# Kernel tuning notes

Hardware: AMD Instinct MI355X
Metric: run time of the kernel (lower is better)

The kernel has to match this reference:

```python
import jax, jax.numpy as jnp
import numpy as np

H = 50   # hidden_dim (hardcoded in module)
D = 16   # input_dim
B = 4096
T = 512

def _uniform(key, shape, k):
    return jax.random.uniform(key, shape, jnp.float32, -k, k)

def setup_inputs() -> dict:
    key = jax.random.key(0)
    ks = jax.random.split(key, 12)
    k = 1.0 / np.sqrt(H)  # PyTorch LSTM/Linear init bound
    return {
        "x": jax.random.normal(ks[0], (B, T, D), jnp.float32),
        "W_ih0": _uniform(ks[1], (4 * H, D), k),
        "W_hh0": _uniform(ks[2], (4 * H, H), k),
        "b_ih0": _uniform(ks[3], (4 * H,), k),
        "b_hh0": _uniform(ks[4], (4 * H,), k),
        "W_ih1": _uniform(ks[5], (4 * H, H), k),
        "W_hh1": _uniform(ks[6], (4 * H, H), k),
        "b_ih1": _uniform(ks[7], (4 * H,), k),
        "b_hh1": _uniform(ks[8], (4 * H,), k),
        "W_fc": _uniform(ks[9], (1, H), k),
        "b_fc": _uniform(ks[10], (1,), k),
    }

def _lstm_layer(x_tbd, W_ih, W_hh, b):
    # x_tbd: [T, B, Din]; returns (ys [T,B,H], h_final [B,H])
    Bsz = x_tbd.shape[1]
    # precompute input projections for all timesteps: [T, B, 4H]
    xproj = jnp.einsum('tbd,gd->tbg', x_tbd, W_ih) + b

    def step(carry, xp):
        h, c = carry
        gates = xp + h @ W_hh.T  # [B, 4H]
        i, f, g, o = jnp.split(gates, 4, axis=-1)  # torch gate order i,f,g,o
        i = jax.nn.sigmoid(i)
        f = jax.nn.sigmoid(f)
        g = jnp.tanh(g)
        o = jax.nn.sigmoid(o)
        c = f * c + i * g
        h = o * jnp.tanh(c)
        return (h, c), h

    init = (jnp.zeros((Bsz, H), x_tbd.dtype), jnp.zeros((Bsz, H), x_tbd.dtype))
    (h_fin, _), ys = jax.lax.scan(step, init, xproj)
    return ys, h_fin

def reference(x, W_ih0, W_hh0, b_ih0, b_hh0, W_ih1, W_hh1, b_ih1, b_hh1, W_fc, b_fc):
    x_tbd = jnp.transpose(x, (1, 0, 2))  # [T, B, D]
    ys0, _ = _lstm_layer(x_tbd, W_ih0, W_hh0, b_ih0 + b_hh0)
    _, h_n = _lstm_layer(ys0, W_ih1, W_hh1, b_ih1 + b_hh1)
    return h_n @ W_fc.T + b_fc  # [B, 1]
```

## Files before the change

kernel.cpp:

```cpp
#include <hip/hip_runtime.h>


#define TSTEPS 512
#define DIN 16
#define HID 50
#define BPB 16

typedef _Float16 half8 __attribute__((ext_vector_type(8)));
typedef __fp16 fp16x2 __attribute__((ext_vector_type(2)));
typedef float f32x4 __attribute__((ext_vector_type(4)));
typedef float f32x2 __attribute__((ext_vector_type(2)));

#define MF(A, B, C) __builtin_amdgcn_mfma_f32_16x16x32_f16((A), (B), (C), 0, 0, 0)

#define HBUF 2304
#define H0_O 0
#define H1_O 4608
#define SH_BYTES 9216

#define BAR() asm volatile("s_waitcnt lgkmcnt(0)\ns_barrier" ::: "memory")

#define NL2E  (-1.4426950408889634f)
#define P2L2E (2.8853900817779268f)

__device__ __forceinline__ unsigned pack2h(float a, float b) {
  union { fp16x2 h; unsigned u; } pk;
  pk.h = __builtin_amdgcn_cvt_pkrtz(a, b);
  return pk.u;
}

__device__ __forceinline__ f32x2 cell2p(const f32x4 gA, const f32x4 gB, f32x2& C) {
  f32x2 gi = {gA[0], gB[0]}, gf = {gA[1], gB[1]};
  f32x2 gg = {gA[2], gB[2]}, go = {gA[3], gB[3]};
  f32x2 ei, ef, eg, eo;
  ei[0] = __builtin_amdgcn_exp2f(gi[0]); ei[1] = __builtin_amdgcn_exp2f(gi[1]);
  ef[0] = __builtin_amdgcn_exp2f(gf[0]); ef[1] = __builtin_amdgcn_exp2f(gf[1]);
  eg[0] = __builtin_amdgcn_exp2f(gg[0]); eg[1] = __builtin_amdgcn_exp2f(gg[1]);
  eo[0] = __builtin_amdgcn_exp2f(go[0]); eo[1] = __builtin_amdgcn_exp2f(go[1]);
  const f32x2 one = {1.f, 1.f};
  const f32x2 c2 = {P2L2E, P2L2E};
  f32x2 a = one + ei, f = one + ef, b = one + eg;
  f32x2 ab = a * b;
  f32x2 f2 = ef * c2 + c2;
  f32x2 t = (eg - one) * f2 + C * ab;
  f32x2 p = f * ab;
  f32x2 rp;
  rp[0] = __builtin_amdgcn_rcpf(p[0]);
  rp[1] = __builtin_amdgcn_rcpf(p[1]);
  C = t * rp;
  f32x2 ec;
  ec[0] = __builtin_amdgcn_exp2f(fminf(C[0], 30.f));
  ec[1] = __builtin_amdgcn_exp2f(fminf(C[1], 30.f));
  f32x2 q = (one + eo) * (one + ec);
  float r2 = __builtin_amdgcn_rcpf(q[0] * q[1]);
  f32x2 h;
  h[0] = (ec[0] - 1.f) * (r2 * q[1]);
  h[1] = (ec[1] - 1.f) * (r2 * q[0]);
  return h;
}

__device__ __forceinline__ half8 load_wfrag(const float* __restrict__ W, int kld,
                                            bool permk, int kreal, int gt, int kt,
                                            int lane, float scale) {
  const int gp = 16 * gt + (lane & 15);
  const int u = gp >> 2, j = gp & 3;
  const int kb = kt * 32 + (lane >> 4) * 8;
  half8 f;
#pragma unroll
  for (int i = 0; i < 8; ++i) {
    const int p = kb + i;
    const int kk = permk ? ((p & ~7) + (((p & 1) << 2) | ((p >> 1) & 3))) : p;
    float v = (u < HID && kk < kreal) ? W[(j * HID + u) * kld + kk] : 0.f;
    f[i] = (_Float16)(v * scale);
  }
  return f;
}

#define LOADX(R0, R1, TT)                                                      \
  do {                                                                         \
    int tl_ = (TT);                                                            \
    if (tl_ > TSTEPS - 1) tl_ = TSTEPS - 1;                                    \
    const float* p_ = xcol + (size_t)tl_ * DIN;                                \
    (R0) = *(const float4*)p_;                                                 \
    (R1) = *(const float4*)(p_ + 4);                                           \
  } while (0)

#define BXB(BX, R0, R1)                                                        \
  do {                                                                         \
    union { half8 h8; fp16x2 p2[4]; } u_;                                      \
    u_.p2[0] = __builtin_amdgcn_cvt_pkrtz((R0).x, (R0).y);                     \
    u_.p2[1] = __builtin_amdgcn_cvt_pkrtz((R0).z, (R0).w);                     \
    u_.p2[2] = __builtin_amdgcn_cvt_pkrtz((R1).x, (R1).y);                     \
    u_.p2[3] = __builtin_amdgcn_cvt_pkrtz((R1).z, (R1).w);                     \
    (BX) = u_.h8;                                                              \
  } while (0)

extern "C" __global__ void __launch_bounds__(512, 2)
lstm2_v11(const float* __restrict__ x,
          const float* __restrict__ Wih0, const float* __restrict__ Whh0,
          const float* __restrict__ bih0, const float* __restrict__ bhh0,
          const float* __restrict__ Wih1, const float* __restrict__ Whh1,
          const float* __restrict__ bih1, const float* __restrict__ bhh1,
          const float* __restrict__ Wfc, const float* __restrict__ bfc,
          float* __restrict__ out) {
  __shared__ __align__(16) char sh[SH_BYTES];
  const int tid = threadIdx.x;
  const int lane = tid & 63;
  const int wv = tid >> 6;
  const int bcol = lane & 15;
  const int kg = lane >> 4;
  const int bbase = blockIdx.x * BPB;

  const int nt = (wv < 5) ? 2 : 1;
  const int gt0 = (wv < 5) ? 2 * wv : (10 + (wv - 5));

  const float* xcol = x + ((size_t)(bbase + bcol)) * TSTEPS * DIN + (kg & 1) * 8;

  for (int i = tid; i < SH_BYTES / 4; i += 512) ((int*)sh)[i] = 0;

  const float wsc = ((lane & 3) == 2) ? P2L2E : NL2E;
  half8 w0x[2], w0h[2][2], w1i[2][2], w1h[2][2];
  f32x4 bias0v[2] = {{0,0,0,0},{0,0,0,0}}, bias1v[2] = {{0,0,0,0},{0,0,0,0}};
#pragma unroll
  for (int gi = 0; gi < 2; ++gi) {
    if (gi < nt) {
      const int gt = gt0 + gi;
      w0x[gi] = load_wfrag(Wih0, DIN, false, DIN, gt, 0, lane, wsc);
#pragma unroll
      for (int kt = 0; kt < 2; ++kt) {
        w0h[gi][kt] = load_wfrag(Whh0, HID, true, HID, gt, kt, lane, wsc);
        w1i[gi][kt] = load_wfrag(Wih1, HID, true, HID, gt, kt, lane, wsc);
        w1h[gi][kt] = load_wfrag(Whh1, HID, true, HID, gt, kt, lane, wsc);
      }
      const int u = 4 * gt + kg;
      if (u < HID) {
#pragma unroll
        for (int j = 0; j < 4; ++j) {
          const float bs = (j == 2) ? P2L2E : NL2E;
          bias0v[gi][j] = bs * (bih0[j * HID + u] + bhh0[j * HID + u]);
          bias1v[gi][j] = bs * (bih1[j * HID + u] + bhh1[j * HID + u]);
        }
      }
    }
  }

  f32x2 C0 = {0.f, 0.f}, C1 = {0.f, 0.f};
  const int hoff = bcol * 144 + kg * 16;
  const int wo = (nt == 2) ? (bcol * 144 + (gt0 >> 1) * 16 + kg * 4)
                           : (bcol * 144 + (8 * (gt0 >> 1) + 2 * kg + (gt0 & 1)) * 2);

  BAR();

  float4 a0, a1, b0, b1;
  LOADX(a0, a1, 0);
  half8 bx0;
  BXB(bx0, a0, a1);
  LOADX(a0, a1, 1);
  LOADX(b0, b1, 2);
  {
    f32x4 r0 = MF(w0x[0], bx0, bias0v[0]);
    if (nt == 2) {
      f32x4 r1 = MF(w0x[1], bx0, bias0v[1]);
      f32x2 H = cell2p(r0, r1, C0);
      *(unsigned*)(sh + H0_O + wo) = pack2h(H[0], H[1]);
    } else {
      f32x2 Cp = {0.f, 0.f};
      f32x2 H = cell2p(r0, r0, Cp);
      *(_Float16*)(sh + H0_O + wo) = (_Float16)H[0];
      C0[0] = 0.f;
      C0[1] = Cp[0];
    }
  }
  BAR();

#define STEP2(P, BX)                                                           \
  do {                                                                         \
    half8 bh0[2], bh1[2];                                                      \
    _Pragma("unroll") for (int kt = 0; kt < 2; ++kt) {                         \
      bh0[kt] = *(const half8*)(sh + H0_O + (P)*HBUF + hoff + kt * 64);        \
      bh1[kt] = *(const half8*)(sh + H1_O + (P)*HBUF + hoff + kt * 64);        \
    }                                                                          \
    const f32x4 z = {0.f, 0.f, 0.f, 0.f};                                      \
    f32x4 tq0a = MF(w1i[0][0], bh0[0], bias1v[0]);                             \
    tq0a = MF(w1h[0][0], bh1[0], tq0a);                                        \
    f32x4 tq0b = MF(w1i[0][1], bh0[1], z);                                     \
    tq0b = MF(w1h[0][1], bh1[1], tq0b);                                        \
    f32x4 qv0 = tq0a + tq0b;                                                   \
    f32x4 tq1a = MF(w1i[1][0], bh0[0], bias1v[1]);                             \
    tq1a = MF(w1h[1][0], bh1[0], tq1a);                                        \
    f32x4 tq1b = MF(w1i[1][1], bh0[1], z);                                     \
    tq1b = MF(w1h[1][1], bh1[1], tq1b);                                        \
    f32x4 qv1 = tq1a + tq1b;                                                   \
    f32x4 tr0a = MF(w0x[0], (BX), bias0v[0]);                                  \
    tr0a = MF(w0h[0][0], bh0[0], tr0a);                                        \
    f32x4 tr0b = MF(w0h[0][1], bh0[1], z);                                     \
    f32x4 rv0 = tr0a + tr0b;                                                   \
    f32x4 tr1a = MF(w0x[1], (BX), bias0v[1]);                                  \
    tr1a = MF(w0h[1][0], bh0[0], tr1a);                                        \
    f32x4 tr1b = MF(w0h[1][1], bh0[1], z);                                     \
    f32x4 rv1 = tr1a + tr1b;                                                   \
    f32x2 H1 = cell2p(qv0, qv1, C1);                                           \
    *(unsigned*)(sh + H1_O + ((P) ^ 1) * HBUF + wo) = pack2h(H1[0], H1[1]);    \
    f32x2 H0 = cell2p(rv0, rv1, C0);                                           \
    *(unsigned*)(sh + H0_O + ((P) ^ 1) * HBUF + wo) = pack2h(H0[0], H0[1]);    \
  } while (0)

#define STEP1(P, BX)                                                           \
  do {                                                                         \
    half8 bh0[2], bh1[2];                                                      \
    _Pragma("unroll") for (int kt = 0; kt < 2; ++kt) {                         \
      bh0[kt] = *(const half8*)(sh + H0_O + (P)*HBUF + hoff + kt * 64);        \
      bh1[kt] = *(const half8*)(sh + H1_O + (P)*HBUF + hoff + kt * 64);        \
    }                                                                          \
    const f32x4 z = {0.f, 0.f, 0.f, 0.f};                                      \
    f32x4 tqa = MF(w1i[0][0], bh0[0], bias1v[0]);                              \
    tqa = MF(w1h[0][0], bh1[0], tqa);                                          \
    f32x4 tqb = MF(w1i[0][1], bh0[1], z);                                      \
    tqb = MF(w1h[0][1], bh1[1], tqb);                                          \
    f32x4 qv = tqa + tqb;                                                      \
    f32x4 tra = MF(w0x[0], (BX), bias0v[0]);                                   \
    tra = MF(w0h[0][0], bh0[0], tra);                                          \
    f32x4 trb = MF(w0h[0][1], bh0[1], z);                                      \
    f32x4 rv = tra + trb;                                                      \
    f32x2 H = cell2p(qv, rv, C0);                                              \
    *(_Float16*)(sh + H1_O + ((P) ^ 1) * HBUF + wo) = (_Float16)H[0];          \
    *(_Float16*)(sh + H0_O + ((P) ^ 1) * HBUF + wo) = (_Float16)H[1];          \
  } while (0)

  for (int s = 0; s < TSTEPS; s += 2) {
    {
      half8 bxA;
      BXB(bxA, a0, a1);
      LOADX(a0, a1, s + 3);
      if (nt == 2) { STEP2(0, bxA); } else { STEP1(0, bxA); }
    }
    BAR();
    {
      half8 bxB;
      BXB(bxB, b0, b1);
      LOADX(b0, b1, s + 4);
      if (nt == 2) { STEP2(1, bxB); } else { STEP1(1, bxB); }
    }
    BAR();
  }

  if (tid < BPB) {
    float acc = bfc[0];
#pragma unroll 10
    for (int u = 0; u < HID; ++u) {
      const int pp = (u & ~7) + 2 * (u & 3) + ((u >> 2) & 1);
      float h = (float)(*(const _Float16*)(sh + H1_O + tid * 144 + pp * 2));
      acc = fmaf(Wfc[u], h, acc);
    }
    out[bbase + tid] = acc;
  }
}

extern "C" void kernel_launch(void* const* d_in, const int* in_sizes, int n_in,
                              void* d_out, int out_size, void* d_ws, size_t ws_size,
                              hipStream_t stream) {
  (void)in_sizes; (void)n_in; (void)d_ws; (void)ws_size; (void)out_size;
  lstm2_v11<<<dim3(4096 / BPB), dim3(512), 0, stream>>>(
      (const float*)d_in[0], (const float*)d_in[1], (const float*)d_in[2],
      (const float*)d_in[3], (const float*)d_in[4], (const float*)d_in[5],
      (const float*)d_in[6], (const float*)d_in[7], (const float*)d_in[8],
      (const float*)d_in[9], (const float*)d_in[10], (float*)d_out);
}
```

Measured before the change: 370.3 us.

## Shrink LSTM block to four waves, each handling three or four gate tiles

Cuts the block from 8 waves to 4. Each wave now owns 3 or 4 gate tiles (wave 0 owns tiles 0-3), so the 13 tiles are covered with fewer waves and the per-step barrier is cheaper. The MFMA accumulation chains are merged into single serial chains instead of split partial sums. In exchange, each wave carries more weight registers and does a longer serial MFMA chain per step, and launch bounds move to 256 threads with 1 block minimum.

```diff
diff --git a/kernel.cpp b/kernel.cpp
--- a/kernel.cpp
+++ b/kernel.cpp
@@ -95,8 +95,8 @@
     (BX) = u_.h8;                                                              \
   } while (0)
 
-extern "C" __global__ void __launch_bounds__(512, 2)
-lstm2_v11(const float* __restrict__ x,
+extern "C" __global__ void __launch_bounds__(256, 1)
+lstm2_v13(const float* __restrict__ x,
           const float* __restrict__ Wih0, const float* __restrict__ Whh0,
           const float* __restrict__ bih0, const float* __restrict__ bhh0,
           const float* __restrict__ Wih1, const float* __restrict__ Whh1,
@@ -111,43 +111,52 @@
   const int kg = lane >> 4;
   const int bbase = blockIdx.x * BPB;
 
-  const int nt = (wv < 5) ? 2 : 1;
-  const int gt0 = (wv < 5) ? 2 * wv : (10 + (wv - 5));
+  const int gA = (wv == 0) ? 0 : (wv == 1) ? 4 : (wv == 2) ? 8 : 10;
+  const int gS = (wv == 1) ? 6 : (wv == 2) ? 7 : 12;
 
   const float* xcol = x + ((size_t)(bbase + bcol)) * TSTEPS * DIN + (kg & 1) * 8;
 
-  for (int i = tid; i < SH_BYTES / 4; i += 512) ((int*)sh)[i] = 0;
+  for (int i = tid; i < SH_BYTES / 4; i += 256) ((int*)sh)[i] = 0;
 
   const float wsc = ((lane & 3) == 2) ? P2L2E : NL2E;
-  half8 w0x[2], w0h[2][2], w1i[2][2], w1h[2][2];
-  f32x4 bias0v[2] = {{0,0,0,0},{0,0,0,0}}, bias1v[2] = {{0,0,0,0},{0,0,0,0}};
-#pragma unroll
-  for (int gi = 0; gi < 2; ++gi) {
-    if (gi < nt) {
-      const int gt = gt0 + gi;
-      w0x[gi] = load_wfrag(Wih0, DIN, false, DIN, gt, 0, lane, wsc);
-#pragma unroll
-      for (int kt = 0; kt < 2; ++kt) {
-        w0h[gi][kt] = load_wfrag(Whh0, HID, true, HID, gt, kt, lane, wsc);
-        w1i[gi][kt] = load_wfrag(Wih1, HID, true, HID, gt, kt, lane, wsc);
-        w1h[gi][kt] = load_wfrag(Whh1, HID, true, HID, gt, kt, lane, wsc);
-      }
-      const int u = 4 * gt + kg;
-      if (u < HID) {
-#pragma unroll
-        for (int j = 0; j < 4; ++j) {
-          const float bs = (j == 2) ? P2L2E : NL2E;
-          bias0v[gi][j] = bs * (bih0[j * HID + u] + bhh0[j * HID + u]);
-          bias1v[gi][j] = bs * (bih1[j * HID + u] + bhh1[j * HID + u]);
+  half8 w0x[4], w0h[4][2], w1i[4][2], w1h[4][2];
+  f32x4 bias0v[4] = {{0,0,0,0},{0,0,0,0},{0,0,0,0},{0,0,0,0}};
+  f32x4 bias1v[4] = {{0,0,0,0},{0,0,0,0},{0,0,0,0},{0,0,0,0}};
+  {
+    int gts[4];
+    gts[0] = gA; gts[1] = gA + 1;
+    gts[2] = (wv == 0) ? 2 : gS;
+    gts[3] = 3;
+    const int nslot = (wv == 0) ? 4 : 3;
+#pragma unroll
+    for (int si = 0; si < 4; ++si) {
+      if (si < nslot) {
+        const int gt = gts[si];
+        w0x[si] = load_wfrag(Wih0, DIN, false, DIN, gt, 0, lane, wsc);
+#pragma unroll
+        for (int kt = 0; kt < 2; ++kt) {
+          w0h[si][kt] = load_wfrag(Whh0, HID, true, HID, gt, kt, lane, wsc);
+          w1i[si][kt] = load_wfrag(Wih1, HID, true, HID, gt, kt, lane, wsc);
+          w1h[si][kt] = load_wfrag(Whh1, HID, true, HID, gt, kt, lane, wsc);
+        }
+        const int u = 4 * gt + kg;
+        if (u < HID) {
+#pragma unroll
+          for (int j = 0; j < 4; ++j) {
+            const float bs = (j == 2) ? P2L2E : NL2E;
+            bias0v[si][j] = bs * (bih0[j * HID + u] + bhh0[j * HID + u]);
+            bias1v[si][j] = bs * (bih1[j * HID + u] + bhh1[j * HID + u]);
+          }
         }
       }
     }
   }
 
-  f32x2 C0 = {0.f, 0.f}, C1 = {0.f, 0.f};
+  f32x2 C0a = {0.f, 0.f}, C1a = {0.f, 0.f}, C0b = {0.f, 0.f}, C1b = {0.f, 0.f};
   const int hoff = bcol * 144 + kg * 16;
-  const int wo = (nt == 2) ? (bcol * 144 + (gt0 >> 1) * 16 + kg * 4)
-                           : (bcol * 144 + (8 * (gt0 >> 1) + 2 * kg + (gt0 & 1)) * 2);
+  const int wo_p1 = bcol * 144 + (gA >> 1) * 16 + kg * 4;
+  const int wo_p2 = bcol * 144 + 16 + kg * 4;
+  const int wo_s  = bcol * 144 + (8 * (gS >> 1) + 2 * kg + (gS & 1)) * 2;
 
   BAR();
 
@@ -159,72 +168,70 @@
   LOADX(b0, b1, 2);
   {
     f32x4 r0 = MF(w0x[0], bx0, bias0v[0]);
-    if (nt == 2) {
-      f32x4 r1 = MF(w0x[1], bx0, bias0v[1]);
-      f32x2 H = cell2p(r0, r1, C0);
-      *(unsigned*)(sh + H0_O + wo) = pack2h(H[0], H[1]);
+    f32x4 r1 = MF(w0x[1], bx0, bias0v[1]);
+    f32x2 H = cell2p(r0, r1, C0a);
+    *(unsigned*)(sh + H0_O + wo_p1) = pack2h(H[0], H[1]);
+    if (wv == 0) {
+      f32x4 r2 = MF(w0x[2], bx0, bias0v[2]);
+      f32x4 r3 = MF(w0x[3], bx0, bias0v[3]);
+      f32x2 H2 = cell2p(r2, r3, C0b);
+      *(unsigned*)(sh + H0_O + wo_p2) = pack2h(H2[0], H2[1]);
     } else {
-      f32x2 Cp = {0.f, 0.f};
-      f32x2 H = cell2p(r0, r0, Cp);
-      *(_Float16*)(sh + H0_O + wo) = (_Float16)H[0];
-      C0[0] = 0.f;
-      C0[1] = Cp[0];
+      f32x4 rs = MF(w0x[2], bx0, bias0v[2]);
+      f32x2 Ct = {0.f, 0.f};
+      f32x2 Hs = cell2p(rs, rs, Ct);
+      *(_Float16*)(sh + H0_O + wo_s) = (_Float16)Hs[0];
+      C0b[0] = 0.f;
+      C0b[1] = Ct[0];
     }
   }
   BAR();
 
-#define STEP2(P, BX)                                                           \
+#define QCHAIN(QV, SI)                                                         \
+  f32x4 QV = MF(w1i[SI][0], bh0[0], bias1v[SI]);                               \
+  QV = MF(w1h[SI][0], bh1[0], QV);                                             \
+  QV = MF(w1i[SI][1], bh0[1], QV);                                             \
+  QV = MF(w1h[SI][1], bh1[1], QV)
+#define RCHAIN(RV, SI, BX)                                                     \
+  f32x4 RV = MF(w0x[SI], (BX), bias0v[SI]);                                    \
+  RV = MF(w0h[SI][0], bh0[0], RV);                                             \
+  RV = MF(w0h[SI][1], bh0[1], RV)
+
+#define STEP(P, BX)                                                            \
   do {                                                                         \
     half8 bh0[2], bh1[2];                                                      \
     _Pragma("unroll") for (int kt = 0; kt < 2; ++kt) {                         \
       bh0[kt] = *(const half8*)(sh + H0_O + (P)*HBUF + hoff + kt * 64);        \
       bh1[kt] = *(const half8*)(sh + H1_O + (P)*HBUF + hoff + kt * 64);        \
     }                                                                          \
-    const f32x4 z = {0.f, 0.f, 0.f, 0.f};                                      \
-    f32x4 tq0a = MF(w1i[0][0], bh0[0], bias1v[0]);                             \
-    tq0a = MF(w1h[0][0], bh1[0], tq0a);                                        \
-    f32x4 tq0b = MF(w1i[0][1], bh0[1], z);                                     \
-    tq0b = MF(w1h[0][1], bh1[1], tq0b);                                        \
-    f32x4 qv0 = tq0a + tq0b;                                                   \
-    f32x4 tq1a = MF(w1i[1][0], bh0[0], bias1v[1]);                             \
-    tq1a = MF(w1h[1][0], bh1[0], tq1a);                                        \
-    f32x4 tq1b = MF(w1i[1][1], bh0[1], z);                                     \
-    tq1b = MF(w1h[1][1], bh1[1], tq1b);                                        \
-    f32x4 qv1 = tq1a + tq1b;                                                   \
-    f32x4 tr0a = MF(w0x[0], (BX), bias0v[0]);                                  \
-    tr0a = MF(w0h[0][0], bh0[0], tr0a);                                        \
-    f32x4 tr0b = MF(w0h[0][1], bh0[1], z);                                     \
-    f32x4 rv0 = tr0a + tr0b;                                                   \
-    f32x4 tr1a = MF(w0x[1], (BX), bias0v[1]);                                  \
-    tr1a = MF(w0h[1][0], bh0[0], tr1a);                                        \
-    f32x4 tr1b = MF(w0h[1][1], bh0[1], z);                                     \
-    f32x4 rv1 = tr1a + tr1b;                                                   \
-    f32x2 H1 = cell2p(qv0, qv1, C1);                                           \
-    *(unsigned*)(sh + H1_O + ((P) ^ 1) * HBUF + wo) = pack2h(H1[0], H1[1]);    \
-    f32x2 H0 = cell2p(rv0, rv1, C0);                                           \
-    *(unsigned*)(sh + H0_O + ((P) ^ 1) * HBUF + wo) = pack2h(H0[0], H0[1]);    \
-  } while (0)
-
-#define STEP1(P, BX)                                                           \
-  do {                                                                         \
-    half8 bh0[2], bh1[2];                                                      \
-    _Pragma("unroll") for (int kt = 0; kt < 2; ++kt) {                         \
-      bh0[kt] = *(const half8*)(sh + H0_O + (P)*HBUF + hoff + kt * 64);        \
-      bh1[kt] = *(const half8*)(sh + H1_O + (P)*HBUF + hoff + kt * 64);        \
+    RCHAIN(rv0, 0, BX);                                                        \
+    RCHAIN(rv1, 1, BX);                                                        \
+    QCHAIN(qv0, 0);                                                            \
+    QCHAIN(qv1, 1);                                                            \
+    if (wv == 0) {                                                             \
+      RCHAIN(rv2, 2, BX);                                                      \
+      RCHAIN(rv3, 3, BX);                                                      \
+      QCHAIN(qv2, 2);                                                          \
+      QCHAIN(qv3, 3);                                                          \
+      f32x2 H0p = cell2p(rv0, rv1, C0a);                                       \
+      *(unsigned*)(sh + H0_O + ((P) ^ 1) * HBUF + wo_p1) = pack2h(H0p[0], H0p[1]); \
+      f32x2 H1p = cell2p(qv0, qv1, C1a);                                       \
+      *(unsigned*)(sh + H1_O + ((P) ^ 1) * HBUF + wo_p1) = pack2h(H1p[0], H1p[1]); \
+      f32x2 H0q = cell2p(rv2, rv3, C0b);                                       \
+      *(unsigned*)(sh + H0_O + ((P) ^ 1) * HBUF + wo_p2) = pack2h(H0q[0], H0q[1]); \
+      f32x2 H1q = cell2p(qv2, qv3, C1b);                                       \
+      *(unsigned*)(sh + H1_O + ((P) ^ 1) * HBUF + wo_p2) = pack2h(H1q[0], H1q[1]); \
+    } else {                                                                   \
+      RCHAIN(rvs, 2, BX);                                                      \
+      QCHAIN(qvs, 2);                                                          \
+      f32x2 H0p = cell2p(rv0, rv1, C0a);                                       \
+      *(unsigned*)(sh + H0_O + ((P) ^ 1) * HBUF + wo_p1) = pack2h(H0p[0], H0p[1]); \
+      f32x2 H1p = cell2p(qv0, qv1, C1a);                                       \
+      *(unsigned*)(sh + H1_O + ((P) ^ 1) * HBUF + wo_p1) = pack2h(H1p[0], H1p[1]); \
+      f32x2 Hs = cell2p(qvs, rvs, C0b);                                        \
+      *(_Float16*)(sh + H1_O + ((P) ^ 1) * HBUF + wo_s) = (_Float16)Hs[0];     \
+      *(_Float16*)(sh + H0_O + ((P) ^ 1) * HBUF + wo_s) = (_Float16)Hs[1];     \
     }                                                                          \
-    const f32x4 z = {0.f, 0.f, 0.f, 0.f};                                      \
-    f32x4 tqa = MF(w1i[0][0], bh0[0], bias1v[0]);                              \
-    tqa = MF(w1h[0][0], bh1[0], tqa);                                          \
-    f32x4 tqb = MF(w1i[0][1], bh0[1], z);                                      \
-    tqb = MF(w1h[0][1], bh1[1], tqb);                                          \
-    f32x4 qv = tqa + tqb;                                                      \
-    f32x4 tra = MF(w0x[0], (BX), bias0v[0]);                                   \
-    tra = MF(w0h[0][0], bh0[0], tra);                                          \
-    f32x4 trb = MF(w0h[0][1], bh0[1], z);                                      \
-    f32x4 rv = tra + trb;                                                      \
-    f32x2 H = cell2p(qv, rv, C0);                                              \
-    *(_Float16*)(sh + H1_O + ((P) ^ 1) * HBUF + wo) = (_Float16)H[0];          \
-    *(_Float16*)(sh + H0_O + ((P) ^ 1) * HBUF + wo) = (_Float16)H[1];          \
   } while (0)
 
   for (int s = 0; s < TSTEPS; s += 2) {
@@ -232,14 +239,14 @@
       half8 bxA;
       BXB(bxA, a0, a1);
       LOADX(a0, a1, s + 3);
-      if (nt == 2) { STEP2(0, bxA); } else { STEP1(0, bxA); }
+      STEP(0, bxA);
     }
     BAR();
     {
       half8 bxB;
       BXB(bxB, b0, b1);
       LOADX(b0, b1, s + 4);
-      if (nt == 2) { STEP2(1, bxB); } else { STEP1(1, bxB); }
+      STEP(1, bxB);
     }
     BAR();
   }
@@ -260,7 +267,7 @@
                               void* d_out, int out_size, void* d_ws, size_t ws_size,
                               hipStream_t stream) {
   (void)in_sizes; (void)n_in; (void)d_ws; (void)ws_size; (void)out_size;
-  lstm2_v11<<<dim3(4096 / BPB), dim3(512), 0, stream>>>(
+  lstm2_v13<<<dim3(4096 / BPB), dim3(256), 0, stream>>>(
       (const float*)d_in[0], (const float*)d_in[1], (const float*)d_in[2],
       (const float*)d_in[3], (const float*)d_in[4], (const float*)d_in[5],
       (const float*)d_in[6], (const float*)d_in[7], (const float*)d_in[8],
```

Result: slower. 389.4 us (+5.2%).
